# Kernel optimization log

Hardware: AMD Instinct MI355X
Metric: run time of the kernel (lower is better)

The kernel has to match this reference:

```python
import jax, jax.numpy as jnp
import numpy as np

N, F_IN, H1, H2, E = 100000, 256, 128, 64, 1600000


def _glorot(key, shape):
    lim = np.sqrt(6.0 / (shape[0] + shape[1]))
    return jax.random.uniform(key, shape, jnp.float32, -lim, lim)


def setup_inputs() -> dict:
    key = jax.random.key(0)
    ks = jax.random.split(key, 8)
    x = jax.random.normal(ks[0], (N, F_IN), jnp.float32)
    edge_index = jax.random.randint(ks[1], (2, E), 0, N, jnp.int64)
    return {
        "x": x,
        "w1": _glorot(ks[2], (F_IN, H1)),
        "b1": jnp.zeros((H1,), jnp.float32),
        "w2": _glorot(ks[3], (H1, H2)),
        "b2": jnp.zeros((H2,), jnp.float32),
        "w3": _glorot(ks[4], (H1, H2)),
        "b3": jnp.zeros((H2,), jnp.float32),
        "edge_index": edge_index,
    }


def _gcn_conv(x, w, b, src, dst, dinv_sqrt):
    # GCNConv: transform first, then symmetric-normalized aggregation with self-loops.
    h = x @ w                                   # [N, out]
    coef = dinv_sqrt[src] * dinv_sqrt[dst]      # [E]
    agg = jnp.zeros_like(h).at[dst].add(h[src] * coef[:, None])
    # self-loop contribution: coefficient deg^-1 per node
    agg = agg + h * (dinv_sqrt * dinv_sqrt)[:, None]
    return agg + b


def reference(x, w1, b1, w2, b2, w3, b3, edge_index):
    src, dst = edge_index[0], edge_index[1]
    n = x.shape[0]
    # degree including self-loop (edge weights all 1)
    deg = jnp.ones((n,), x.dtype).at[dst].add(1.0)
    dinv_sqrt = jax.lax.rsqrt(deg)
    hidden = jax.nn.relu(_gcn_conv(x, w1, b1, src, dst, dinv_sqrt))
    mu = _gcn_conv(hidden, w2, b2, src, dst, dinv_sqrt)
    logvar = _gcn_conv(hidden, w3, b3, src, dst, dinv_sqrt)
    return (mu, logvar)
```

## Files before the change

### kernel.cpp

```cpp
#include <hip/hip_runtime.h>


#define TPB 256
#define GSHIFT 9
#define GSIZE 512
#define PART_M 8192

typedef __attribute__((ext_vector_type(8))) short short8;
typedef __attribute__((ext_vector_type(4))) short short4v;
typedef __attribute__((ext_vector_type(4))) float floatx4;
typedef __attribute__((ext_vector_type(4))) unsigned int uint4v;

__device__ __forceinline__ void split2(float v, short& hi, short& lo) {
    unsigned u = __float_as_uint(v);
    float hf = __uint_as_float(u & 0xFFFF0000u);
    float lf = v - hf;
    hi = (short)(u >> 16);
    lo = (short)(__float_as_uint(lf) >> 16);
}

__device__ __forceinline__ short bf16_rtn(float v) {
    unsigned u = __float_as_uint(v);
    u += 0x7FFF + ((u >> 16) & 1);
    return (short)(u >> 16);
}

__device__ __forceinline__ void addrow(float* a, uint4v v) {
    a[0] += __uint_as_float(v[0] << 16); a[1] += __uint_as_float(v[0] & 0xFFFF0000u);
    a[2] += __uint_as_float(v[1] << 16); a[3] += __uint_as_float(v[1] & 0xFFFF0000u);
    a[4] += __uint_as_float(v[2] << 16); a[5] += __uint_as_float(v[2] & 0xFFFF0000u);
    a[6] += __uint_as_float(v[3] << 16); a[7] += __uint_as_float(v[3] & 0xFFFF0000u);
}

__device__ __forceinline__ void gload_lds16(const void* g, void* l) {
    __builtin_amdgcn_global_load_lds(
        (const __attribute__((address_space(1))) unsigned int*)g,
        (__attribute__((address_space(3))) unsigned int*)l, 16, 0, 0);
}

__global__ __launch_bounds__(TPB) void group_count(const int* __restrict__ dst,
                                                   int* __restrict__ ghist, int E) {
    __shared__ int h[256];
    int t = threadIdx.x;
    h[t] = 0;
    __syncthreads();
    int stride = gridDim.x * TPB;
    for (int k = blockIdx.x * TPB + t; k < E; k += stride)
        atomicAdd(&h[dst[k] >> GSHIFT], 1);
    __syncthreads();
    if (h[t]) atomicAdd(&ghist[t], h[t]);
}

__global__ __launch_bounds__(256) void goff_scan(const int* __restrict__ ghist,
                                                 int* __restrict__ goff, int ngrp) {
    __shared__ int sc[256];
    int t = threadIdx.x;
    int v = (t < ngrp) ? ghist[t] : 0;
    sc[t] = v;
    __syncthreads();
#pragma unroll
    for (int off = 1; off < 256; off <<= 1) {
        int x = (t >= off) ? sc[t - off] : 0;
        __syncthreads();
        sc[t] += x;
        __syncthreads();
    }
    goff[t] = sc[t] - v;
    if (t == 255) goff[256] = sc[255];
}

__global__ __launch_bounds__(256) void partition_kernel(const int* __restrict__ src,
                                                        const int* __restrict__ dst,
                                                        const int* __restrict__ goff,
                                                        int* __restrict__ gcur,
                                                        int* __restrict__ staged, int E) {
    __shared__ int sorted[PART_M];
    __shared__ int sc[256];
    __shared__ int lstart[257];
    __shared__ int cur[256];
    __shared__ int gb[256];
    int t = threadIdx.x;
    int base = blockIdx.x * PART_M;
    int mloc = min(PART_M, E - base);

    sc[t] = 0;
    cur[t] = 0;
    __syncthreads();
    for (int k = t; k < mloc; k += 256)
        atomicAdd(&sc[dst[base + k] >> GSHIFT], 1);
    __syncthreads();
    int v = sc[t];
    __syncthreads();
    sc[t] = v;
    __syncthreads();
#pragma unroll
    for (int off = 1; off < 256; off <<= 1) {
        int x = (t >= off) ? sc[t - off] : 0;
        __syncthreads();
        sc[t] += x;
        __syncthreads();
    }
    lstart[t] = sc[t] - v;
    if (t == 255) lstart[256] = sc[255];
    gb[t] = goff[t] + atomicAdd(&gcur[t], v);
    __syncthreads();
    for (int k = t; k < mloc; k += 256) {
        int d = dst[base + k];
        int s = src[base + k];
        int b = d >> GSHIFT;
        int pos = lstart[b] + atomicAdd(&cur[b], 1);
        sorted[pos] = (s << GSHIFT) | (d & (GSIZE - 1));
    }
    __syncthreads();
    for (int e = t; e < mloc; e += 256) {
        int lo = 0, hi = 256;
        while (hi - lo > 1) {
            int mid = (lo + hi) >> 1;
            if (lstart[mid] <= e) lo = mid; else hi = mid;
        }
        staged[gb[lo] + (e - lstart[lo])] = sorted[e];
    }
}

__global__ __launch_bounds__(512) void build_csr(const int* __restrict__ staged,
                                                 const int* __restrict__ goff,
                                                 int* __restrict__ cnt,
                                                 float* __restrict__ dinv,
                                                 int* __restrict__ rowptr,
                                                 int* __restrict__ csr, int N) {
    __shared__ int hist[512];
    __shared__ int sc[512];
    __shared__ int lrow[512];
    __shared__ int cur[512];
    int t = threadIdx.x;
    int g = blockIdx.x;
    int s0 = goff[g], s1 = goff[g + 1];
    hist[t] = 0;
    cur[t] = 0;
    __syncthreads();
    for (int k = s0 + t; k < s1; k += 512)
        atomicAdd(&hist[staged[k] & (GSIZE - 1)], 1);
    __syncthreads();
    int v = hist[t];
    sc[t] = v;
    __syncthreads();
#pragma unroll
    for (int off = 1; off < 512; off <<= 1) {
        int x = (t >= off) ? sc[t - off] : 0;
        __syncthreads();
        sc[t] += x;
        __syncthreads();
    }
    int rp = s0 + sc[t] - v;
    lrow[t] = rp;
    int node = (g << GSHIFT) + t;
    if (node < N) {
        rowptr[node] = rp;
        cnt[node] = v;
        dinv[node] = rsqrtf(1.0f + (float)v);
    }
    __syncthreads();
    for (int k = s0 + t; k < s1; k += 512) {
        int p = staged[k];
        int dl = p & (GSIZE - 1);
        int pos = lrow[dl] + atomicAdd(&cur[dl], 1);
        csr[pos] = p >> GSHIFT;
    }
}

__global__ void prep_w1t(const float* __restrict__ w1, short* __restrict__ th,
                         short* __restrict__ tl) {
    int t = blockIdx.x * TPB + threadIdx.x;
    int k = t & 255, n = t >> 8;
    float v = w1[(size_t)k * 128 + n];
    short h, l;
    split2(v, h, l);
    th[t] = h;
    tl[t] = l;
}

__global__ void prep_wcatt(const float* __restrict__ w2, const float* __restrict__ b2,
                           const float* __restrict__ w3, const float* __restrict__ b3,
                           short* __restrict__ th, short* __restrict__ tl,
                           float* __restrict__ bcat) {
    int t = blockIdx.x * TPB + threadIdx.x;
    int k = t & 127, n = t >> 7;
    float v = (n < 64) ? w2[(size_t)k * 64 + n] : w3[(size_t)k * 64 + (n - 64)];
    short h, l;
    split2(v, h, l);
    th[t] = h;
    tl[t] = l;
    if (t < 64) { bcat[t] = b2[t]; bcat[64 + t] = b3[t]; }
}

__global__ __launch_bounds__(TPB) void gemm_mfma_f32in(const float* __restrict__ A,
                                                       const short* __restrict__ Bth,
                                                       const short* __restrict__ Btl,
                                                       const float* __restrict__ rs,
                                                       short* __restrict__ Cb, int M, int K) {
    __shared__ float Af[2][64 * 32];
    __shared__ short Bh[2][128 * 32];
    __shared__ short Bl[2][128 * 32];
    int t = threadIdx.x;
    int wave = t >> 6, lane = t & 63, quad = lane >> 4, l16 = lane & 15;
    int bm0 = blockIdx.x * 64;

    floatx4 acc[8];
#pragma unroll
    for (int nt = 0; nt < 8; ++nt) acc[nt] = (floatx4){0.f, 0.f, 0.f, 0.f};

    auto stage = [&](int pb, int k0) {
#pragma unroll
        for (int i = 0; i < 2; ++i) {
            int g = i * 256 + t;
            int row = g >> 3, col = g & 7;
            int gr = bm0 + row;
            if (gr >= M) gr = M - 1;
            int scol = col ^ (row & 7);
            gload_lds16(A + (size_t)gr * K + k0 + scol * 4,
                        &Af[pb][(i * 256 + wave * 64) * 4]);
        }
#pragma unroll
        for (int i = 0; i < 2; ++i) {
            int g = i * 256 + t;
            int row = g >> 2, col = g & 3;
            int scol = col ^ ((row >> 1) & 3);
            size_t off = (size_t)row * K + k0 + scol * 8;
            int lb = (i * 256 + wave * 64) * 8;
            gload_lds16(Bth + off, &Bh[pb][lb]);
            gload_lds16(Btl + off, &Bl[pb][lb]);
        }
    };

    int nk = K >> 5;
    stage(0, 0);
    __syncthreads();
    int am = wave * 16 + l16;
    int ac0 = ((quad * 2 + 0) ^ (am & 7)) * 4;
    int ac1 = ((quad * 2 + 1) ^ (am & 7)) * 4;
    int bc = (quad ^ ((l16 >> 1) & 3)) * 8;
    for (int ks = 0; ks < nk; ++ks) {
        int pb = ks & 1;
        if (ks + 1 < nk) stage(pb ^ 1, (ks + 1) << 5);
        float4 fa0 = *(const float4*)&Af[pb][am * 32 + ac0];
        float4 fa1 = *(const float4*)&Af[pb][am * 32 + ac1];
        short8 a_h, a_l;
        {
            short h, l;
            split2(fa0.x, h, l); a_h[0] = h; a_l[0] = l;
            split2(fa0.y, h, l); a_h[1] = h; a_l[1] = l;
            split2(fa0.z, h, l); a_h[2] = h; a_l[2] = l;
            split2(fa0.w, h, l); a_h[3] = h; a_l[3] = l;
            split2(fa1.x, h, l); a_h[4] = h; a_l[4] = l;
            split2(fa1.y, h, l); a_h[5] = h; a_l[5] = l;
            split2(fa1.z, h, l); a_h[6] = h; a_l[6] = l;
            split2(fa1.w, h, l); a_h[7] = h; a_l[7] = l;
        }
#pragma unroll
        for (int nt = 0; nt < 8; ++nt) {
            int bn = nt * 16 + l16;
            short8 b_h = *(const short8*)&Bh[pb][bn * 32 + bc];
            short8 b_l = *(const short8*)&Bl[pb][bn * 32 + bc];
            acc[nt] = __builtin_amdgcn_mfma_f32_16x16x32_bf16(a_l, b_h, acc[nt], 0, 0, 0);
            acc[nt] = __builtin_amdgcn_mfma_f32_16x16x32_bf16(a_h, b_l, acc[nt], 0, 0, 0);
            acc[nt] = __builtin_amdgcn_mfma_f32_16x16x32_bf16(a_h, b_h, acc[nt], 0, 0, 0);
        }
        __syncthreads();
    }
#pragma unroll
    for (int reg = 0; reg < 4; ++reg) {
        int gr = bm0 + wave * 16 + quad * 4 + reg;
        if (gr < M) {
            float s = rs[gr];
            short* cp = Cb + (size_t)gr * 128;
#pragma unroll
            for (int nt = 0; nt < 8; ++nt) cp[nt * 16 + l16] = bf16_rtn(acc[nt][reg] * s);
        }
    }
}

__global__ __launch_bounds__(TPB) void gemm_mfma_bfin(const short* __restrict__ AH,
                                                      const short* __restrict__ AL,
                                                      const short* __restrict__ Bth,
                                                      const short* __restrict__ Btl,
                                                      const float* __restrict__ rs,
                                                      short* __restrict__ Cb, int M, int K) {
    __shared__ short Ah[2][64 * 32], Al[2][64 * 32];
    __shared__ short Bh[2][128 * 32], Bl[2][128 * 32];
    int t = threadIdx.x;
    int wave = t >> 6, lane = t & 63, quad = lane >> 4, l16 = lane & 15;
    int bm0 = blockIdx.x * 64;

    floatx4 acc[8];
#pragma unroll
    for (int nt = 0; nt < 8; ++nt) acc[nt] = (floatx4){0.f, 0.f, 0.f, 0.f};

    auto stage = [&](int pb, int k0) {
        {
            int row = t >> 2, col = t & 3;
            int gr = bm0 + row;
            if (gr >= M) gr = M - 1;
            int scol = col ^ ((row >> 1) & 3);
            size_t off = (size_t)gr * K + k0 + scol * 8;
            int lb = (wave * 64) * 8;
            gload_lds16(AH + off, &Ah[pb][lb]);
            gload_lds16(AL + off, &Al[pb][lb]);
        }
#pragma unroll
        for (int i = 0; i < 2; ++i) {
            int g = i * 256 + t;
            int row = g >> 2, col = g & 3;
            int scol = col ^ ((row >> 1) & 3);
            size_t off = (size_t)row * K + k0 + scol * 8;
            int lb = (i * 256 + wave * 64) * 8;
            gload_lds16(Bth + off, &Bh[pb][lb]);
            gload_lds16(Btl + off, &Bl[pb][lb]);
        }
    };

    int nk = K >> 5;
    stage(0, 0);
    __syncthreads();
    int am = wave * 16 + l16;
    int ac = (quad ^ ((am >> 1) & 3)) * 8;
    int bc = (quad ^ ((l16 >> 1) & 3)) * 8;
    for (int ks = 0; ks < nk; ++ks) {
        int pb = ks & 1;
        if (ks + 1 < nk) stage(pb ^ 1, (ks + 1) << 5);
        short8 a_h = *(const short8*)&Ah[pb][am * 32 + ac];
        short8 a_l = *(const short8*)&Al[pb][am * 32 + ac];
#pragma unroll
        for (int nt = 0; nt < 8; ++nt) {
            int bn = nt * 16 + l16;
            short8 b_h = *(const short8*)&Bh[pb][bn * 32 + bc];
            short8 b_l = *(const short8*)&Bl[pb][bn * 32 + bc];
            acc[nt] = __builtin_amdgcn_mfma_f32_16x16x32_bf16(a_l, b_h, acc[nt], 0, 0, 0);
            acc[nt] = __builtin_amdgcn_mfma_f32_16x16x32_bf16(a_h, b_l, acc[nt], 0, 0, 0);
            acc[nt] = __builtin_amdgcn_mfma_f32_16x16x32_bf16(a_h, b_h, acc[nt], 0, 0, 0);
        }
        __syncthreads();
    }
#pragma unroll
    for (int reg = 0; reg < 4; ++reg) {
        int gr = bm0 + wave * 16 + quad * 4 + reg;
        if (gr < M) {
            float s = rs[gr];
            short* cp = Cb + (size_t)gr * 128;
#pragma unroll
            for (int nt = 0; nt < 8; ++nt) cp[nt * 16 + l16] = bf16_rtn(acc[nt][reg] * s);
        }
    }
}

__global__ __launch_bounds__(TPB) void gather_hidden(const int* __restrict__ csr,
                                                     const int* __restrict__ rowptr,
                                                     const int* __restrict__ cnt,
                                                     const float* __restrict__ dinv,
                                                     const short* __restrict__ hs,
                                                     const float* __restrict__ b1,
                                                     short* __restrict__ hidH,
                                                     short* __restrict__ hidL, int N) {
    size_t t = (size_t)blockIdx.x * TPB + threadIdx.x;
    int nid = (int)(t >> 4);
    int lane = threadIdx.x & 15;
    if (nid >= N) return;
    int start = rowptr[nid];
    int deg = cnt[nid];
    const uint4v* hp = (const uint4v*)hs;
    float acc[8] = {0, 0, 0, 0, 0, 0, 0, 0};
    addrow(acc, __builtin_nontemporal_load(&hp[(size_t)nid * 16 + lane]));
    int j = 0;
    for (; j + 3 < deg; j += 4) {
        int s0 = csr[start + j], s1 = csr[start + j + 1];
        int s2 = csr[start + j + 2], s3 = csr[start + j + 3];
        uint4v v0 = hp[(size_t)s0 * 16 + lane];
        uint4v v1 = hp[(size_t)s1 * 16 + lane];
        uint4v v2 = hp[(size_t)s2 * 16 + lane];
        uint4v v3 = hp[(size_t)s3 * 16 + lane];
        addrow(acc, v0);
        addrow(acc, v1);
        addrow(acc, v2);
        addrow(acc, v3);
    }
    if (j + 1 < deg) {
        int s0 = csr[start + j], s1 = csr[start + j + 1];
        uint4v v0 = hp[(size_t)s0 * 16 + lane];
        uint4v v1 = hp[(size_t)s1 * 16 + lane];
        addrow(acc, v0);
        addrow(acc, v1);
        j += 2;
    }
    if (j < deg) addrow(acc, hp[(size_t)csr[start + j] * 16 + lane]);
    float di = dinv[nid];
    float4 b0 = ((const float4*)b1)[lane * 2];
    float4 b1v = ((const float4*)b1)[lane * 2 + 1];
    float bb[8] = {b0.x, b0.y, b0.z, b0.w, b1v.x, b1v.y, b1v.z, b1v.w};
    unsigned hiw[8];
    short low[8];
#pragma unroll
    for (int i = 0; i < 8; ++i) {
        float h = fmaxf(fmaf(di, acc[i], bb[i]), 0.f);
        unsigned u = __float_as_uint(h);
        hiw[i] = u >> 16;
        float hf = __uint_as_float(u & 0xFFFF0000u);
        low[i] = bf16_rtn(h - hf);
    }
    uint4v ph, pl;
    ph[0] = hiw[0] | (hiw[1] << 16);
    ph[1] = hiw[2] | (hiw[3] << 16);
    ph[2] = hiw[4] | (hiw[5] << 16);
    ph[3] = hiw[6] | (hiw[7] << 16);
    pl[0] = (unsigned short)low[0] | ((unsigned)(unsigned short)low[1] << 16);
    pl[1] = (unsigned short)low[2] | ((unsigned)(unsigned short)low[3] << 16);
    pl[2] = (unsigned short)low[4] | ((unsigned)(unsigned short)low[5] << 16);
    pl[3] = (unsigned short)low[6] | ((unsigned)(unsigned short)low[7] << 16);
    __builtin_nontemporal_store(ph, &((uint4v*)hidH)[(size_t)nid * 16 + lane]);
    __builtin_nontemporal_store(pl, &((uint4v*)hidL)[(size_t)nid * 16 + lane]);
}

__global__ __launch_bounds__(TPB) void gather_out(const int* __restrict__ csr,
                                                  const int* __restrict__ rowptr,
                                                  const int* __restrict__ cnt,
                                                  const float* __restrict__ dinv,
                                                  const short* __restrict__ hs,
                                                  const float* __restrict__ bcat,
                                                  float* __restrict__ out, int N) {
    size_t t = (size_t)blockIdx.x * TPB + threadIdx.x;
    int nid = (int)(t >> 4);
    int lane = threadIdx.x & 15;
    if (nid >= N) return;
    int start = rowptr[nid];
    int deg = cnt[nid];
    const uint4v* hp = (const uint4v*)hs;
    float acc[8] = {0, 0, 0, 0, 0, 0, 0, 0};
    addrow(acc, __builtin_nontemporal_load(&hp[(size_t)nid * 16 + lane]));
    int j = 0;
    for (; j + 3 < deg; j += 4) {
        int s0 = csr[start + j], s1 = csr[start + j + 1];
        int s2 = csr[start + j + 2], s3 = csr[start + j + 3];
        uint4v v0 = hp[(size_t)s0 * 16 + lane];
        uint4v v1 = hp[(size_t)s1 * 16 + lane];
        uint4v v2 = hp[(size_t)s2 * 16 + lane];
        uint4v v3 = hp[(size_t)s3 * 16 + lane];
        addrow(acc, v0);
        addrow(acc, v1);
        addrow(acc, v2);
        addrow(acc, v3);
    }
    if (j + 1 < deg) {
        int s0 = csr[start + j], s1 = csr[start + j + 1];
        uint4v v0 = hp[(size_t)s0 * 16 + lane];
        uint4v v1 = hp[(size_t)s1 * 16 + lane];
        addrow(acc, v0);
        addrow(acc, v1);
        j += 2;
    }
    if (j < deg) addrow(acc, hp[(size_t)csr[start + j] * 16 + lane]);
    float di = dinv[nid];
    float4 b0 = ((const float4*)bcat)[lane * 2];
    float4 b1v = ((const float4*)bcat)[lane * 2 + 1];
    floatx4 r0, r1;
    r0[0] = fmaf(di, acc[0], b0.x);
    r0[1] = fmaf(di, acc[1], b0.y);
    r0[2] = fmaf(di, acc[2], b0.z);
    r0[3] = fmaf(di, acc[3], b0.w);
    r1[0] = fmaf(di, acc[4], b1v.x);
    r1[1] = fmaf(di, acc[5], b1v.y);
    r1[2] = fmaf(di, acc[6], b1v.z);
    r1[3] = fmaf(di, acc[7], b1v.w);
    int f = lane * 8;
    float* dp = (f < 64) ? (out + (size_t)nid * 64 + f)
                         : (out + (size_t)N * 64 + (size_t)nid * 64 + (f - 64));
    __builtin_nontemporal_store(r0, (floatx4*)dp);
    __builtin_nontemporal_store(r1, (floatx4*)(dp + 4));
}

extern "C" void kernel_launch(void* const* d_in, const int* in_sizes, int n_in,
                              void* d_out, int out_size, void* d_ws, size_t ws_size,
                              hipStream_t stream) {
    const float* x  = (const float*)d_in[0];
    const float* w1 = (const float*)d_in[1];
    const float* b1 = (const float*)d_in[2];
    const float* w2 = (const float*)d_in[3];
    const float* b2 = (const float*)d_in[4];
    const float* w3 = (const float*)d_in[5];
    const float* b3 = (const float*)d_in[6];
    const int*   ei = (const int*)d_in[7];

    const int N = in_sizes[0] / 256;
    const int E = in_sizes[7] / 2;
    const int K1 = 256;

    float* out = (float*)d_out;

    size_t nh = (size_t)N * 128;
    short* hs1    = (short*)d_ws;
    short* hidH   = hs1 + nh;
    short* hidL   = hidH + nh;
    short* hs2    = hidL + nh;
    int*   cnt    = (int*)(hs2 + nh);
    float* dinv   = (float*)(cnt + N);
    int*   rowptr = (int*)(dinv + N);
    int*   cursor = rowptr + N;
    int*   bsum   = cursor + N;
    float* bcat   = (float*)(bsum + 512);
    short* w1t_h  = (short*)(bcat + 128);
    short* w1t_l  = w1t_h + 128 * 256;
    short* wct_h  = w1t_l + 128 * 256;
    short* wct_l  = wct_h + 128 * 128;
    int*   csr    = (int*)(wct_l + 128 * 128);

    const int* srcp = ei;
    const int* dstp = ei + E;

    const int ngrp = (N + GSIZE - 1) >> GSHIFT;
    int* ghist  = cursor;
    int* gcur   = cursor + 256;
    int* goff   = cursor + 512;
    int* staged = (int*)hs2;

    hipMemsetAsync(cursor, 0, 512 * sizeof(int), stream);

    int gc_blocks = (E + TPB * 16 - 1) / (TPB * 16);
    group_count<<<gc_blocks, TPB, 0, stream>>>(dstp, ghist, E);
    goff_scan<<<1, 256, 0, stream>>>(ghist, goff, ngrp);
    partition_kernel<<<(E + PART_M - 1) / PART_M, 256, 0, stream>>>(srcp, dstp, goff, gcur,
                                                                    staged, E);
    build_csr<<<ngrp, 512, 0, stream>>>(staged, goff, cnt, dinv, rowptr, csr, N);

    prep_w1t<<<(128 * 256) / TPB, TPB, 0, stream>>>(w1, w1t_h, w1t_l);
    prep_wcatt<<<(128 * 128) / TPB, TPB, 0, stream>>>(w2, b2, w3, b3, wct_h, wct_l, bcat);

    gemm_mfma_f32in<<<(N + 63) / 64, TPB, 0, stream>>>(x, w1t_h, w1t_l, dinv, hs1, N, K1);

    size_t gthreads = (size_t)N * 16;
    gather_hidden<<<(unsigned)((gthreads + TPB - 1) / TPB), TPB, 0, stream>>>(
        csr, rowptr, cnt, dinv, hs1, b1, hidH, hidL, N);

    gemm_mfma_bfin<<<(N + 63) / 64, TPB, 0, stream>>>(hidH, hidL, wct_h, wct_l, dinv, hs2, N, 128);

    gather_out<<<(unsigned)((gthreads + TPB - 1) / TPB), TPB, 0, stream>>>(
        csr, rowptr, cnt, dinv, hs2, bcat, out, N);
}
```

Measured before the change: 432.2 us.

## Fuse layer-1 neighbor gather into second-layer GEMM via shared-memory hidden tile

Measured after the change: 460.0 us. +6.5%, slower.

```diff
diff --git a/kernel.cpp b/kernel.cpp
--- a/kernel.cpp
+++ b/kernel.cpp
@@ -30,6 +30,33 @@
     a[2] += __uint_as_float(v[1] << 16); a[3] += __uint_as_float(v[1] & 0xFFFF0000u);
     a[4] += __uint_as_float(v[2] << 16); a[5] += __uint_as_float(v[2] & 0xFFFF0000u);
     a[6] += __uint_as_float(v[3] << 16); a[7] += __uint_as_float(v[3] & 0xFFFF0000u);
+}
+
+__device__ __forceinline__ void gather_accum(float* acc, const int* __restrict__ csr,
+                                             int start, int deg, const uint4v* hp,
+                                             int lane) {
+    int j = 0;
+    for (; j + 3 < deg; j += 4) {
+        int s0 = csr[start + j], s1 = csr[start + j + 1];
+        int s2 = csr[start + j + 2], s3 = csr[start + j + 3];
+        uint4v v0 = hp[(size_t)s0 * 16 + lane];
+        uint4v v1 = hp[(size_t)s1 * 16 + lane];
+        uint4v v2 = hp[(size_t)s2 * 16 + lane];
+        uint4v v3 = hp[(size_t)s3 * 16 + lane];
+        addrow(acc, v0);
+        addrow(acc, v1);
+        addrow(acc, v2);
+        addrow(acc, v3);
+    }
+    if (j + 1 < deg) {
+        int s0 = csr[start + j], s1 = csr[start + j + 1];
+        uint4v v0 = hp[(size_t)s0 * 16 + lane];
+        uint4v v1 = hp[(size_t)s1 * 16 + lane];
+        addrow(acc, v0);
+        addrow(acc, v1);
+        j += 2;
+    }
+    if (j < deg) addrow(acc, hp[(size_t)csr[start + j] * 16 + lane]);
 }
 
 __device__ __forceinline__ void gload_lds16(const void* g, void* l) {
@@ -279,143 +306,112 @@
     }
 }
 
-__global__ __launch_bounds__(TPB) void gemm_mfma_bfin(const short* __restrict__ AH,
-                                                      const short* __restrict__ AL,
-                                                      const short* __restrict__ Bth,
-                                                      const short* __restrict__ Btl,
-                                                      const float* __restrict__ rs,
-                                                      short* __restrict__ Cb, int M, int K) {
-    __shared__ short Ah[2][64 * 32], Al[2][64 * 32];
+__global__ __launch_bounds__(TPB) void gather_gemm2(const int* __restrict__ csr,
+                                                    const int* __restrict__ rowptr,
+                                                    const int* __restrict__ cnt,
+                                                    const float* __restrict__ dinv,
+                                                    const short* __restrict__ hs,
+                                                    const float* __restrict__ b1,
+                                                    const short* __restrict__ Bth,
+                                                    const short* __restrict__ Btl,
+                                                    short* __restrict__ Cb, int N) {
+    __shared__ short Ah[64 * 128], Al[64 * 128];
     __shared__ short Bh[2][128 * 32], Bl[2][128 * 32];
     int t = threadIdx.x;
     int wave = t >> 6, lane = t & 63, quad = lane >> 4, l16 = lane & 15;
     int bm0 = blockIdx.x * 64;
 
-    floatx4 acc[8];
-#pragma unroll
-    for (int nt = 0; nt < 8; ++nt) acc[nt] = (floatx4){0.f, 0.f, 0.f, 0.f};
-
-    auto stage = [&](int pb, int k0) {
-        {
-            int row = t >> 2, col = t & 3;
-            int gr = bm0 + row;
-            if (gr >= M) gr = M - 1;
-            int scol = col ^ ((row >> 1) & 3);
-            size_t off = (size_t)gr * K + k0 + scol * 8;
-            int lb = (wave * 64) * 8;
-            gload_lds16(AH + off, &Ah[pb][lb]);
-            gload_lds16(AL + off, &Al[pb][lb]);
-        }
+    auto stageB = [&](int pb, int k0) {
 #pragma unroll
         for (int i = 0; i < 2; ++i) {
             int g = i * 256 + t;
             int row = g >> 2, col = g & 3;
             int scol = col ^ ((row >> 1) & 3);
-            size_t off = (size_t)row * K + k0 + scol * 8;
+            size_t off = (size_t)row * 128 + k0 + scol * 8;
             int lb = (i * 256 + wave * 64) * 8;
             gload_lds16(Bth + off, &Bh[pb][lb]);
             gload_lds16(Btl + off, &Bl[pb][lb]);
         }
     };
 
-    int nk = K >> 5;
-    stage(0, 0);
-    __syncthreads();
+    stageB(0, 0);
+
+    {
+        const uint4v* hp = (const uint4v*)hs;
+        int nrow = t >> 4;
+        float4 c0 = ((const float4*)b1)[l16 * 2];
+        float4 c1 = ((const float4*)b1)[l16 * 2 + 1];
+        float bb[8] = {c0.x, c0.y, c0.z, c0.w, c1.x, c1.y, c1.z, c1.w};
+#pragma unroll
+        for (int sw = 0; sw < 4; ++sw) {
+            int r = sw * 16 + nrow;
+            int nid = bm0 + r;
+            int nc = (nid < N) ? nid : N - 1;
+            int start = rowptr[nc];
+            int deg = cnt[nc];
+            float acc[8] = {0, 0, 0, 0, 0, 0, 0, 0};
+            addrow(acc, __builtin_nontemporal_load(&hp[(size_t)nc * 16 + l16]));
+            gather_accum(acc, csr, start, deg, hp, l16);
+            float di = dinv[nc];
+            unsigned hiw[8];
+            short low[8];
+#pragma unroll
+            for (int i = 0; i < 8; ++i) {
+                float h = fmaxf(fmaf(di, acc[i], bb[i]), 0.f);
+                unsigned u = __float_as_uint(h);
+                hiw[i] = u >> 16;
+                float hf = __uint_as_float(u & 0xFFFF0000u);
+                low[i] = bf16_rtn(h - hf);
+            }
+            uint4v ph, pl;
+            ph[0] = hiw[0] | (hiw[1] << 16);
+            ph[1] = hiw[2] | (hiw[3] << 16);
+            ph[2] = hiw[4] | (hiw[5] << 16);
+            ph[3] = hiw[6] | (hiw[7] << 16);
+            pl[0] = (unsigned short)low[0] | ((unsigned)(unsigned short)low[1] << 16);
+            pl[1] = (unsigned short)low[2] | ((unsigned)(unsigned short)low[3] << 16);
+            pl[2] = (unsigned short)low[4] | ((unsigned)(unsigned short)low[5] << 16);
+            pl[3] = (unsigned short)low[6] | ((unsigned)(unsigned short)low[7] << 16);
+            int slot = l16 ^ (r & 7);
+            *(uint4v*)&Ah[r * 128 + slot * 8] = ph;
+            *(uint4v*)&Al[r * 128 + slot * 8] = pl;
+        }
+    }
+    __syncthreads();
+
+    floatx4 acc2[8];
+#pragma unroll
+    for (int nt = 0; nt < 8; ++nt) acc2[nt] = (floatx4){0.f, 0.f, 0.f, 0.f};
     int am = wave * 16 + l16;
-    int ac = (quad ^ ((am >> 1) & 3)) * 8;
     int bc = (quad ^ ((l16 >> 1) & 3)) * 8;
-    for (int ks = 0; ks < nk; ++ks) {
+    for (int ks = 0; ks < 4; ++ks) {
         int pb = ks & 1;
-        if (ks + 1 < nk) stage(pb ^ 1, (ks + 1) << 5);
-        short8 a_h = *(const short8*)&Ah[pb][am * 32 + ac];
-        short8 a_l = *(const short8*)&Al[pb][am * 32 + ac];
+        if (ks + 1 < 4) stageB(pb ^ 1, (ks + 1) * 32);
+        int c = ks * 4 + quad;
+        int slot = c ^ (am & 7);
+        short8 a_h = *(const short8*)&Ah[am * 128 + slot * 8];
+        short8 a_l = *(const short8*)&Al[am * 128 + slot * 8];
 #pragma unroll
         for (int nt = 0; nt < 8; ++nt) {
             int bn = nt * 16 + l16;
             short8 b_h = *(const short8*)&Bh[pb][bn * 32 + bc];
             short8 b_l = *(const short8*)&Bl[pb][bn * 32 + bc];
-            acc[nt] = __builtin_amdgcn_mfma_f32_16x16x32_bf16(a_l, b_h, acc[nt], 0, 0, 0);
-            acc[nt] = __builtin_amdgcn_mfma_f32_16x16x32_bf16(a_h, b_l, acc[nt], 0, 0, 0);
-            acc[nt] = __builtin_amdgcn_mfma_f32_16x16x32_bf16(a_h, b_h, acc[nt], 0, 0, 0);
+            acc2[nt] = __builtin_amdgcn_mfma_f32_16x16x32_bf16(a_l, b_h, acc2[nt], 0, 0, 0);
+            acc2[nt] = __builtin_amdgcn_mfma_f32_16x16x32_bf16(a_h, b_l, acc2[nt], 0, 0, 0);
+            acc2[nt] = __builtin_amdgcn_mfma_f32_16x16x32_bf16(a_h, b_h, acc2[nt], 0, 0, 0);
         }
         __syncthreads();
     }
 #pragma unroll
     for (int reg = 0; reg < 4; ++reg) {
         int gr = bm0 + wave * 16 + quad * 4 + reg;
-        if (gr < M) {
-            float s = rs[gr];
+        if (gr < N) {
+            float s = dinv[gr];
             short* cp = Cb + (size_t)gr * 128;
 #pragma unroll
-            for (int nt = 0; nt < 8; ++nt) cp[nt * 16 + l16] = bf16_rtn(acc[nt][reg] * s);
-        }
-    }
-}
-
-__global__ __launch_bounds__(TPB) void gather_hidden(const int* __restrict__ csr,
-                                                     const int* __restrict__ rowptr,
-                                                     const int* __restrict__ cnt,
-                                                     const float* __restrict__ dinv,
-                                                     const short* __restrict__ hs,
-                                                     const float* __restrict__ b1,
-                                                     short* __restrict__ hidH,
-                                                     short* __restrict__ hidL, int N) {
-    size_t t = (size_t)blockIdx.x * TPB + threadIdx.x;
-    int nid = (int)(t >> 4);
-    int lane = threadIdx.x & 15;
-    if (nid >= N) return;
-    int start = rowptr[nid];
-    int deg = cnt[nid];
-    const uint4v* hp = (const uint4v*)hs;
-    float acc[8] = {0, 0, 0, 0, 0, 0, 0, 0};
-    addrow(acc, __builtin_nontemporal_load(&hp[(size_t)nid * 16 + lane]));
-    int j = 0;
-    for (; j + 3 < deg; j += 4) {
-        int s0 = csr[start + j], s1 = csr[start + j + 1];
-        int s2 = csr[start + j + 2], s3 = csr[start + j + 3];
-        uint4v v0 = hp[(size_t)s0 * 16 + lane];
-        uint4v v1 = hp[(size_t)s1 * 16 + lane];
-        uint4v v2 = hp[(size_t)s2 * 16 + lane];
-        uint4v v3 = hp[(size_t)s3 * 16 + lane];
-        addrow(acc, v0);
-        addrow(acc, v1);
-        addrow(acc, v2);
-        addrow(acc, v3);
-    }
-    if (j + 1 < deg) {
-        int s0 = csr[start + j], s1 = csr[start + j + 1];
-        uint4v v0 = hp[(size_t)s0 * 16 + lane];
-        uint4v v1 = hp[(size_t)s1 * 16 + lane];
-        addrow(acc, v0);
-        addrow(acc, v1);
-        j += 2;
-    }
-    if (j < deg) addrow(acc, hp[(size_t)csr[start + j] * 16 + lane]);
-    float di = dinv[nid];
-    float4 b0 = ((const float4*)b1)[lane * 2];
-    float4 b1v = ((const float4*)b1)[lane * 2 + 1];
-    float bb[8] = {b0.x, b0.y, b0.z, b0.w, b1v.x, b1v.y, b1v.z, b1v.w};
-    unsigned hiw[8];
-    short low[8];
-#pragma unroll
-    for (int i = 0; i < 8; ++i) {
-        float h = fmaxf(fmaf(di, acc[i], bb[i]), 0.f);
-        unsigned u = __float_as_uint(h);
-        hiw[i] = u >> 16;
-        float hf = __uint_as_float(u & 0xFFFF0000u);
-        low[i] = bf16_rtn(h - hf);
-    }
-    uint4v ph, pl;
-    ph[0] = hiw[0] | (hiw[1] << 16);
-    ph[1] = hiw[2] | (hiw[3] << 16);
-    ph[2] = hiw[4] | (hiw[5] << 16);
-    ph[3] = hiw[6] | (hiw[7] << 16);
-    pl[0] = (unsigned short)low[0] | ((unsigned)(unsigned short)low[1] << 16);
-    pl[1] = (unsigned short)low[2] | ((unsigned)(unsigned short)low[3] << 16);
-    pl[2] = (unsigned short)low[4] | ((unsigned)(unsigned short)low[5] << 16);
-    pl[3] = (unsigned short)low[6] | ((unsigned)(unsigned short)low[7] << 16);
-    __builtin_nontemporal_store(ph, &((uint4v*)hidH)[(size_t)nid * 16 + lane]);
-    __builtin_nontemporal_store(pl, &((uint4v*)hidL)[(size_t)nid * 16 + lane]);
+            for (int nt = 0; nt < 8; ++nt) cp[nt * 16 + l16] = bf16_rtn(acc2[nt][reg] * s);
+        }
+    }
 }
 
 __global__ __launch_bounds__(TPB) void gather_out(const int* __restrict__ csr,
@@ -434,28 +430,7 @@
     const uint4v* hp = (const uint4v*)hs;
     float acc[8] = {0, 0, 0, 0, 0, 0, 0, 0};
     addrow(acc, __builtin_nontemporal_load(&hp[(size_t)nid * 16 + lane]));
-    int j = 0;
-    for (; j + 3 < deg; j += 4) {
-        int s0 = csr[start + j], s1 = csr[start + j + 1];
-        int s2 = csr[start + j + 2], s3 = csr[start + j + 3];
-        uint4v v0 = hp[(size_t)s0 * 16 + lane];
-        uint4v v1 = hp[(size_t)s1 * 16 + lane];
-        uint4v v2 = hp[(size_t)s2 * 16 + lane];
-        uint4v v3 = hp[(size_t)s3 * 16 + lane];
-        addrow(acc, v0);
-        addrow(acc, v1);
-        addrow(acc, v2);
-        addrow(acc, v3);
-    }
-    if (j + 1 < deg) {
-        int s0 = csr[start + j], s1 = csr[start + j + 1];
-        uint4v v0 = hp[(size_t)s0 * 16 + lane];
-        uint4v v1 = hp[(size_t)s1 * 16 + lane];
-        addrow(acc, v0);
-        addrow(acc, v1);
-        j += 2;
-    }
-    if (j < deg) addrow(acc, hp[(size_t)csr[start + j] * 16 + lane]);
+    gather_accum(acc, csr, start, deg, hp, lane);
     float di = dinv[nid];
     float4 b0 = ((const float4*)bcat)[lane * 2];
     float4 b1v = ((const float4*)bcat)[lane * 2 + 1];
@@ -495,9 +470,7 @@
 
     size_t nh = (size_t)N * 128;
     short* hs1    = (short*)d_ws;
-    short* hidH   = hs1 + nh;
-    short* hidL   = hidH + nh;
-    short* hs2    = hidL + nh;
+    short* hs2    = hs1 + 3 * nh;
     int*   cnt    = (int*)(hs2 + nh);
     float* dinv   = (float*)(cnt + N);
     int*   rowptr = (int*)(dinv + N);
@@ -533,12 +506,10 @@
 
     gemm_mfma_f32in<<<(N + 63) / 64, TPB, 0, stream>>>(x, w1t_h, w1t_l, dinv, hs1, N, K1);
 
+    gather_gemm2<<<(N + 63) / 64, TPB, 0, stream>>>(csr, rowptr, cnt, dinv, hs1, b1,
+                                                    wct_h, wct_l, hs2, N);
+
     size_t gthreads = (size_t)N * 16;
-    gather_hidden<<<(unsigned)((gthreads + TPB - 1) / TPB), TPB, 0, stream>>>(
-        csr, rowptr, cnt, dinv, hs1, b1, hidH, hidL, N);
-
-    gemm_mfma_bfin<<<(N + 63) / 64, TPB, 0, stream>>>(hidH, hidL, wct_h, wct_l, dinv, hs2, N, 128);
-
     gather_out<<<(unsigned)((gthreads + TPB - 1) / TPB), TPB, 0, stream>>>(
         csr, rowptr, cnt, dinv, hs2, bcat, out, N);
 }
```

## Merge prep and scan kernels, vectorize edge reads in partitioning

Applied to the files above, without the earlier changes.

Result: no change. 425.7 us (-1.5%).

```diff
diff --git a/kernel.cpp b/kernel.cpp
--- a/kernel.cpp
+++ b/kernel.cpp
@@ -32,41 +32,114 @@
     a[6] += __uint_as_float(v[3] << 16); a[7] += __uint_as_float(v[3] & 0xFFFF0000u);
 }
 
+__device__ __forceinline__ void gather_accum(float* acc, const int* __restrict__ csr,
+                                             int start, int deg, const uint4v* hp,
+                                             int lane) {
+    int j = 0;
+    for (; j + 3 < deg; j += 4) {
+        int s0 = csr[start + j], s1 = csr[start + j + 1];
+        int s2 = csr[start + j + 2], s3 = csr[start + j + 3];
+        uint4v v0 = hp[(size_t)s0 * 16 + lane];
+        uint4v v1 = hp[(size_t)s1 * 16 + lane];
+        uint4v v2 = hp[(size_t)s2 * 16 + lane];
+        uint4v v3 = hp[(size_t)s3 * 16 + lane];
+        addrow(acc, v0);
+        addrow(acc, v1);
+        addrow(acc, v2);
+        addrow(acc, v3);
+    }
+    if (j + 1 < deg) {
+        int s0 = csr[start + j], s1 = csr[start + j + 1];
+        uint4v v0 = hp[(size_t)s0 * 16 + lane];
+        uint4v v1 = hp[(size_t)s1 * 16 + lane];
+        addrow(acc, v0);
+        addrow(acc, v1);
+        j += 2;
+    }
+    if (j < deg) addrow(acc, hp[(size_t)csr[start + j] * 16 + lane]);
+}
+
 __device__ __forceinline__ void gload_lds16(const void* g, void* l) {
     __builtin_amdgcn_global_load_lds(
         (const __attribute__((address_space(1))) unsigned int*)g,
         (__attribute__((address_space(3))) unsigned int*)l, 16, 0, 0);
 }
 
+__global__ __launch_bounds__(TPB) void prep_all(const float* __restrict__ w1,
+                                                const float* __restrict__ w2,
+                                                const float* __restrict__ b2,
+                                                const float* __restrict__ w3,
+                                                const float* __restrict__ b3,
+                                                short* __restrict__ w1t_h,
+                                                short* __restrict__ w1t_l,
+                                                short* __restrict__ wct_h,
+                                                short* __restrict__ wct_l,
+                                                float* __restrict__ bcat,
+                                                int* __restrict__ cursor) {
+    int b = blockIdx.x, t0 = threadIdx.x;
+    if (b < 128) {
+        int t = b * TPB + t0;
+        int k = t & 255, n = t >> 8;
+        float v = w1[(size_t)k * 128 + n];
+        short h, l;
+        split2(v, h, l);
+        w1t_h[t] = h;
+        w1t_l[t] = l;
+    } else if (b < 192) {
+        int t = (b - 128) * TPB + t0;
+        int k = t & 127, n = t >> 7;
+        float v = (n < 64) ? w2[(size_t)k * 64 + n] : w3[(size_t)k * 64 + (n - 64)];
+        short h, l;
+        split2(v, h, l);
+        wct_h[t] = h;
+        wct_l[t] = l;
+        if (t < 64) { bcat[t] = b2[t]; bcat[64 + t] = b3[t]; }
+    } else {
+        for (int i = t0; i < 513; i += TPB) cursor[i] = 0;
+    }
+}
+
 __global__ __launch_bounds__(TPB) void group_count(const int* __restrict__ dst,
-                                                   int* __restrict__ ghist, int E) {
+                                                   int* __restrict__ cursor, int E) {
+    int* ghist = cursor;
+    int* done  = cursor + 512;
+    int* goff  = cursor + 513;
     __shared__ int h[256];
+    __shared__ int lastFlag;
     int t = threadIdx.x;
     h[t] = 0;
     __syncthreads();
+    const int4* d4 = (const int4*)dst;
+    int E4 = E >> 2;
     int stride = gridDim.x * TPB;
-    for (int k = blockIdx.x * TPB + t; k < E; k += stride)
+    for (int k = blockIdx.x * TPB + t; k < E4; k += stride) {
+        int4 v = d4[k];
+        atomicAdd(&h[v.x >> GSHIFT], 1);
+        atomicAdd(&h[v.y >> GSHIFT], 1);
+        atomicAdd(&h[v.z >> GSHIFT], 1);
+        atomicAdd(&h[v.w >> GSHIFT], 1);
+    }
+    for (int k = (E4 << 2) + blockIdx.x * TPB + t; k < E; k += stride)
         atomicAdd(&h[dst[k] >> GSHIFT], 1);
     __syncthreads();
     if (h[t]) atomicAdd(&ghist[t], h[t]);
-}
-
-__global__ __launch_bounds__(256) void goff_scan(const int* __restrict__ ghist,
-                                                 int* __restrict__ goff, int ngrp) {
-    __shared__ int sc[256];
-    int t = threadIdx.x;
-    int v = (t < ngrp) ? ghist[t] : 0;
-    sc[t] = v;
+    __threadfence();
+    __syncthreads();
+    if (t == 0) lastFlag = (atomicAdd(done, 1) == (int)gridDim.x - 1);
+    __syncthreads();
+    if (!lastFlag) return;
+    int v = atomicAdd(&ghist[t], 0);
+    h[t] = v;
     __syncthreads();
 #pragma unroll
     for (int off = 1; off < 256; off <<= 1) {
-        int x = (t >= off) ? sc[t - off] : 0;
-        __syncthreads();
-        sc[t] += x;
-        __syncthreads();
-    }
-    goff[t] = sc[t] - v;
-    if (t == 255) goff[256] = sc[255];
+        int x = (t >= off) ? h[t - off] : 0;
+        __syncthreads();
+        h[t] += x;
+        __syncthreads();
+    }
+    goff[t] = h[t] - v;
+    if (t == 255) goff[256] = h[255];
 }
 
 __global__ __launch_bounds__(256) void partition_kernel(const int* __restrict__ src,
@@ -82,11 +155,21 @@
     int t = threadIdx.x;
     int base = blockIdx.x * PART_M;
     int mloc = min(PART_M, E - base);
+    int m4 = mloc >> 2;
 
     sc[t] = 0;
     cur[t] = 0;
     __syncthreads();
-    for (int k = t; k < mloc; k += 256)
+    const int4* d4 = (const int4*)(dst + base);
+    const int4* s4 = (const int4*)(src + base);
+    for (int k = t; k < m4; k += 256) {
+        int4 v = d4[k];
+        atomicAdd(&sc[v.x >> GSHIFT], 1);
+        atomicAdd(&sc[v.y >> GSHIFT], 1);
+        atomicAdd(&sc[v.z >> GSHIFT], 1);
+        atomicAdd(&sc[v.w >> GSHIFT], 1);
+    }
+    for (int k = (m4 << 2) + t; k < mloc; k += 256)
         atomicAdd(&sc[dst[base + k] >> GSHIFT], 1);
     __syncthreads();
     int v = sc[t];
@@ -104,12 +187,23 @@
     if (t == 255) lstart[256] = sc[255];
     gb[t] = goff[t] + atomicAdd(&gcur[t], v);
     __syncthreads();
-    for (int k = t; k < mloc; k += 256) {
+    for (int k = t; k < m4; k += 256) {
+        int4 dv = d4[k];
+        int4 sv = s4[k];
+        int b0 = dv.x >> GSHIFT;
+        sorted[lstart[b0] + atomicAdd(&cur[b0], 1)] = (sv.x << GSHIFT) | (dv.x & (GSIZE - 1));
+        int b1 = dv.y >> GSHIFT;
+        sorted[lstart[b1] + atomicAdd(&cur[b1], 1)] = (sv.y << GSHIFT) | (dv.y & (GSIZE - 1));
+        int b2 = dv.z >> GSHIFT;
+        sorted[lstart[b2] + atomicAdd(&cur[b2], 1)] = (sv.z << GSHIFT) | (dv.z & (GSIZE - 1));
+        int b3 = dv.w >> GSHIFT;
+        sorted[lstart[b3] + atomicAdd(&cur[b3], 1)] = (sv.w << GSHIFT) | (dv.w & (GSIZE - 1));
+    }
+    for (int k = (m4 << 2) + t; k < mloc; k += 256) {
         int d = dst[base + k];
         int s = src[base + k];
         int b = d >> GSHIFT;
-        int pos = lstart[b] + atomicAdd(&cur[b], 1);
-        sorted[pos] = (s << GSHIFT) | (d & (GSIZE - 1));
+        sorted[lstart[b] + atomicAdd(&cur[b], 1)] = (s << GSHIFT) | (d & (GSIZE - 1));
     }
     __syncthreads();
     for (int e = t; e < mloc; e += 256) {
@@ -166,31 +260,6 @@
         int pos = lrow[dl] + atomicAdd(&cur[dl], 1);
         csr[pos] = p >> GSHIFT;
     }
-}
-
-__global__ void prep_w1t(const float* __restrict__ w1, short* __restrict__ th,
-                         short* __restrict__ tl) {
-    int t = blockIdx.x * TPB + threadIdx.x;
-    int k = t & 255, n = t >> 8;
-    float v = w1[(size_t)k * 128 + n];
-    short h, l;
-    split2(v, h, l);
-    th[t] = h;
-    tl[t] = l;
-}
-
-__global__ void prep_wcatt(const float* __restrict__ w2, const float* __restrict__ b2,
-                           const float* __restrict__ w3, const float* __restrict__ b3,
-                           short* __restrict__ th, short* __restrict__ tl,
-                           float* __restrict__ bcat) {
-    int t = blockIdx.x * TPB + threadIdx.x;
-    int k = t & 127, n = t >> 7;
-    float v = (n < 64) ? w2[(size_t)k * 64 + n] : w3[(size_t)k * 64 + (n - 64)];
-    short h, l;
-    split2(v, h, l);
-    th[t] = h;
-    tl[t] = l;
-    if (t < 64) { bcat[t] = b2[t]; bcat[64 + t] = b3[t]; }
 }
 
 __global__ __launch_bounds__(TPB) void gemm_mfma_f32in(const float* __restrict__ A,
@@ -369,28 +438,7 @@
     const uint4v* hp = (const uint4v*)hs;
     float acc[8] = {0, 0, 0, 0, 0, 0, 0, 0};
     addrow(acc, __builtin_nontemporal_load(&hp[(size_t)nid * 16 + lane]));
-    int j = 0;
-    for (; j + 3 < deg; j += 4) {
-        int s0 = csr[start + j], s1 = csr[start + j + 1];
-        int s2 = csr[start + j + 2], s3 = csr[start + j + 3];
-        uint4v v0 = hp[(size_t)s0 * 16 + lane];
-        uint4v v1 = hp[(size_t)s1 * 16 + lane];
-        uint4v v2 = hp[(size_t)s2 * 16 + lane];
-        uint4v v3 = hp[(size_t)s3 * 16 + lane];
-        addrow(acc, v0);
-        addrow(acc, v1);
-        addrow(acc, v2);
-        addrow(acc, v3);
-    }
-    if (j + 1 < deg) {
-        int s0 = csr[start + j], s1 = csr[start + j + 1];
-        uint4v v0 = hp[(size_t)s0 * 16 + lane];
-        uint4v v1 = hp[(size_t)s1 * 16 + lane];
-        addrow(acc, v0);
-        addrow(acc, v1);
-        j += 2;
-    }
-    if (j < deg) addrow(acc, hp[(size_t)csr[start + j] * 16 + lane]);
+    gather_accum(acc, csr, start, deg, hp, lane);
     float di = dinv[nid];
     float4 b0 = ((const float4*)b1)[lane * 2];
     float4 b1v = ((const float4*)b1)[lane * 2 + 1];
@@ -434,28 +482,7 @@
     const uint4v* hp = (const uint4v*)hs;
     float acc[8] = {0, 0, 0, 0, 0, 0, 0, 0};
     addrow(acc, __builtin_nontemporal_load(&hp[(size_t)nid * 16 + lane]));
-    int j = 0;
-    for (; j + 3 < deg; j += 4) {
-        int s0 = csr[start + j], s1 = csr[start + j + 1];
-        int s2 = csr[start + j + 2], s3 = csr[start + j + 3];
-        uint4v v0 = hp[(size_t)s0 * 16 + lane];
-        uint4v v1 = hp[(size_t)s1 * 16 + lane];
-        uint4v v2 = hp[(size_t)s2 * 16 + lane];
-        uint4v v3 = hp[(size_t)s3 * 16 + lane];
-        addrow(acc, v0);
-        addrow(acc, v1);
-        addrow(acc, v2);
-        addrow(acc, v3);
-    }
-    if (j + 1 < deg) {
-        int s0 = csr[start + j], s1 = csr[start + j + 1];
-        uint4v v0 = hp[(size_t)s0 * 16 + lane];
-        uint4v v1 = hp[(size_t)s1 * 16 + lane];
-        addrow(acc, v0);
-        addrow(acc, v1);
-        j += 2;
-    }
-    if (j < deg) addrow(acc, hp[(size_t)csr[start + j] * 16 + lane]);
+    gather_accum(acc, csr, start, deg, hp, lane);
     float di = dinv[nid];
     float4 b0 = ((const float4*)bcat)[lane * 2];
     float4 b1v = ((const float4*)bcat)[lane * 2 + 1];
@@ -514,23 +541,19 @@
     const int* dstp = ei + E;
 
     const int ngrp = (N + GSIZE - 1) >> GSHIFT;
-    int* ghist  = cursor;
     int* gcur   = cursor + 256;
-    int* goff   = cursor + 512;
+    int* goff   = cursor + 513;
     int* staged = (int*)hs2;
 
-    hipMemsetAsync(cursor, 0, 512 * sizeof(int), stream);
-
-    int gc_blocks = (E + TPB * 16 - 1) / (TPB * 16);
-    group_count<<<gc_blocks, TPB, 0, stream>>>(dstp, ghist, E);
-    goff_scan<<<1, 256, 0, stream>>>(ghist, goff, ngrp);
+    prep_all<<<193, TPB, 0, stream>>>(w1, w2, b2, w3, b3, w1t_h, w1t_l, wct_h, wct_l,
+                                      bcat, cursor);
+
+    int gc_blocks = ((E >> 2) + TPB * 4 - 1) / (TPB * 4);
+    group_count<<<gc_blocks, TPB, 0, stream>>>(dstp, cursor, E);
     partition_kernel<<<(E + PART_M - 1) / PART_M, 256, 0, stream>>>(srcp, dstp, goff, gcur,
                                                                     staged, E);
     build_csr<<<ngrp, 512, 0, stream>>>(staged, goff, cnt, dinv, rowptr, csr, N);
 
-    prep_w1t<<<(128 * 256) / TPB, TPB, 0, stream>>>(w1, w1t_h, w1t_l);
-    prep_wcatt<<<(128 * 128) / TPB, TPB, 0, stream>>>(w2, b2, w3, b3, wct_h, wct_l, bcat);
-
     gemm_mfma_f32in<<<(N + 63) / 64, TPB, 0, stream>>>(x, w1t_h, w1t_l, dinv, hs1, N, K1);
 
     size_t gthreads = (size_t)N * 16;
```
